# Performance work log

Measured on AMD Instinct MI355X. Metric: run time of the kernel, lower is better.

Reference implementation:

```python
import jax, jax.numpy as jnp
import numpy as np

S, B, H2 = 2048, 16, 1024   # seq_len, batch, 2*hidden_dim
H = H2 // 2                  # hidden_dim
N = 4096                     # number of spans with nonempty tags
T = 8192                     # total number of target tags (ragged, flattened)
L = 256                      # label_dim
V = 50000                    # vocab size
GAMMA = 1.0


def setup_inputs() -> dict:
    key = jax.random.key(0)
    ks = jax.random.split(key, 10)
    hidden = jax.random.normal(ks[0], (S, B, H2), jnp.float32)
    W1 = jax.random.normal(ks[1], (L, H2), jnp.float32) * (1.0 / np.sqrt(H2))
    b1 = jnp.zeros((L,), jnp.float32)
    W2 = jax.random.normal(ks[2], (V, L), jnp.float32) * (1.0 / np.sqrt(L))
    b2 = jnp.zeros((V,), jnp.float32)
    span_bid = jax.random.randint(ks[3], (N,), 0, B, jnp.int32)
    span_begin = jax.random.randint(ks[4], (N,), 0, S, jnp.int32)
    span_end = jax.random.randint(ks[5], (N,), 0, S, jnp.int32)
    tag_span_id = jax.random.randint(ks[6], (T,), 0, N, jnp.int32)
    tags = jax.random.randint(ks[7], (T,), 0, V, jnp.int32)
    return {"hidden": hidden, "W1": W1, "b1": b1, "W2": W2, "b2": b2,
            "span_bid": span_bid, "span_begin": span_begin,
            "span_end": span_end, "tag_span_id": tag_span_id, "tags": tags}


def reference(hidden, W1, b1, W2, b2, span_bid, span_begin, span_end,
              tag_span_id, tags):
    # span embedding: forward half at begin-1 (wraps like torch negative idx),
    # backward half at end.  -> [N, 2H]
    fwd = hidden[(span_begin - 1) % S, span_bid, :H]
    bwd = hidden[span_end, span_bid, H:]
    feat = jnp.concatenate([fwd, bwd], axis=-1)          # [N, 2H]
    x = jnp.tanh(feat @ W1.T + b1)                       # [N, L]  (Linear+Tanh)
    logits = x @ W2.T + b2                               # [N, V]
    logp = jax.nn.log_softmax(logits, axis=-1)           # stable softmax->log
    pos_logp = logp[tag_span_id, tags]                   # [T] gathered targets
    pos = jnp.exp(pos_logp)                              # positive_probs
    # focal loss, gamma=1: -(1-p)^gamma * log(p), summed over all tags
    loss = jnp.sum(-((1.0 - pos) ** GAMMA) * pos_logp)
    loss = loss / (jnp.float32(T) + 1e-5)
    return loss.reshape(1)
```

## Files before the change

kernel.cpp:

```cpp
#include <hip/hip_runtime.h>
#include <hip/hip_fp8.h>

#define S_    2048
#define B_    16
#define H2_   1024
#define H_    512
#define N_    4096
#define T_    8192
#define L_    256
#define V_    50000
#define VPAD_ 50048

#define LOG2E_ 1.44269504088896f

typedef float  floatx4 __attribute__((ext_vector_type(4)));
typedef __bf16 bf16x8  __attribute__((ext_vector_type(8)));
typedef int    intx4   __attribute__((ext_vector_type(4)));
typedef int    intx8   __attribute__((ext_vector_type(8)));

__device__ inline unsigned short f2bf(float f) {
  unsigned u = __builtin_bit_cast(unsigned, f);
  unsigned r = u + 0x7fffu + ((u >> 16) & 1u);
  return (unsigned short)(r >> 16);
}
__device__ inline float bf2f(unsigned short s) {
  unsigned u = ((unsigned)s) << 16;
  return __builtin_bit_cast(float, u);
}
__device__ inline unsigned char f2fp8(float f) {
  return (unsigned char)__hip_cvt_float_to_fp8(f, __HIP_SATFINITE, __HIP_E4M3);
}

__device__ inline void stage16(const void* g, void* l) {
  __builtin_amdgcn_global_load_lds(
      (const __attribute__((address_space(1))) void*)g,
      (__attribute__((address_space(3))) void*)l, 16, 0, 0);
}

__global__ __launch_bounds__(256) void gather_k(
    const float* __restrict__ hidden, const int* __restrict__ sbid,
    const int* __restrict__ sbeg, const int* __restrict__ send,
    unsigned short* __restrict__ featbf, float* __restrict__ lse) {
  const int n = blockIdx.x;
  const int t = threadIdx.x;
  if (t == 0) lse[n] = 0.f;
  if (n == 0 && t == 1) lse[N_] = 0.f;
  if (n == 0 && t == 2) ((unsigned*)lse)[N_ + 1] = 0u;
  const int bid = sbid[n];
  int r = sbeg[n] - 1; if (r < 0) r += S_;
  const int e = send[n];
  const size_t fbase = (size_t)r * (B_ * H2_) + (size_t)bid * H2_;
  const size_t bbase = (size_t)e * (B_ * H2_) + (size_t)bid * H2_;
  const int c = t * 4;
  const float4 v = (t < 128) ? *reinterpret_cast<const float4*>(hidden + fbase + c)
                             : *reinterpret_cast<const float4*>(hidden + bbase + c);
  unsigned short o[4];
  o[0] = f2bf(v.x); o[1] = f2bf(v.y); o[2] = f2bf(v.z); o[3] = f2bf(v.w);
  *reinterpret_cast<unsigned long long*>(featbf + (size_t)n * H2_ + c) =
      *reinterpret_cast<unsigned long long*>(o);
}

__global__ __launch_bounds__(256) void convert_k(
    const float* __restrict__ W1, const float* __restrict__ W2,
    const float* __restrict__ b2, unsigned short* __restrict__ w1b,
    unsigned char* __restrict__ w2f8, float* __restrict__ ebp) {
  const int gid = blockIdx.x * 256 + threadIdx.x;
  const int gstride = gridDim.x * 256;
  for (long j = (long)gid * 8; j < (long)VPAD_ * 256; j += (long)gstride * 8) {
    int row = (int)(j >> 8);
    unsigned char o[8];
    if (row < V_) {
#pragma unroll
      for (int q = 0; q < 8; q++) o[q] = f2fp8(W2[j + q] * LOG2E_);
    } else {
#pragma unroll
      for (int q = 0; q < 8; q++) o[q] = 0;
    }
    *reinterpret_cast<unsigned long long*>(w2f8 + j) =
        *reinterpret_cast<unsigned long long*>(o);
  }
  for (int j = gid; j < L_ * H2_; j += gstride) w1b[j] = f2bf(W1[j]);
  for (int j = gid; j < VPAD_; j += gstride) ebp[j] = (j < V_) ? __expf(b2[j]) : 0.f;
}

__global__ __launch_bounds__(256) void gemm1_k(
    const unsigned short* __restrict__ A,
    const unsigned short* __restrict__ Bw,
    const float* __restrict__ b1,
    unsigned short* __restrict__ xbf,
    unsigned char* __restrict__ xf8) {
  __shared__ __align__(16) unsigned short sA[64 * 64];
  __shared__ __align__(16) unsigned short sB[64 * 64];
  const int tid   = threadIdx.x;
  const int mtile = (int)(blockIdx.x >> 2) * 64;
  const int ntile = (int)(blockIdx.x & 3) * 64;
  const int lane = tid & 63, wave = tid >> 6;
  const int wr = (wave & 1) * 32, wc = (wave >> 1) * 32;
  const int fr = lane & 15, fq = lane >> 4;
  floatx4 acc[2][2] = {};
  for (int k0 = 0; k0 < H2_; k0 += 64) {
#pragma unroll
    for (int i = 0; i < 2; i++) {
      const int slot = tid + i * 256;
      const int r = slot >> 3, cc = slot & 7;
      const int gk = cc ^ (r & 7);
      stage16(A  + (size_t)(mtile + r) * H2_ + k0 + gk * 8, &sA[slot * 8]);
      stage16(Bw + (size_t)(ntile + r) * H2_ + k0 + gk * 8, &sB[slot * 8]);
    }
    __syncthreads();
#pragma unroll
    for (int ks = 0; ks < 2; ks++) {
      bf16x8 av[2], bv[2];
#pragma unroll
      for (int mi = 0; mi < 2; mi++) {
        const int r = wr + mi * 16 + fr, kc = ks * 4 + fq;
        av[mi] = *reinterpret_cast<const bf16x8*>(&sA[(r * 8 + (kc ^ (r & 7))) * 8]);
      }
#pragma unroll
      for (int ni = 0; ni < 2; ni++) {
        const int r = wc + ni * 16 + fr, kc = ks * 4 + fq;
        bv[ni] = *reinterpret_cast<const bf16x8*>(&sB[(r * 8 + (kc ^ (r & 7))) * 8]);
      }
#pragma unroll
      for (int mi = 0; mi < 2; mi++)
#pragma unroll
        for (int ni = 0; ni < 2; ni++)
          acc[mi][ni] = __builtin_amdgcn_mfma_f32_16x16x32_bf16(av[mi], bv[ni], acc[mi][ni], 0, 0, 0);
    }
    __syncthreads();
  }
#pragma unroll
  for (int ni = 0; ni < 2; ni++) {
    const int col = ntile + wc + ni * 16 + fr;
    const float bias = b1[col];
#pragma unroll
    for (int mi = 0; mi < 2; mi++)
#pragma unroll
      for (int r = 0; r < 4; r++) {
        const int row = mtile + wr + mi * 16 + fq * 4 + r;
        const float t = tanhf(acc[mi][ni][r] + bias);
        xbf[(size_t)row * L_ + col] = f2bf(t);
        xf8[(size_t)row * L_ + col] = f2fp8(t);
      }
  }
}

__global__ __launch_bounds__(512, 4) void gemm2_k(
    const unsigned char* __restrict__ X8,
    const unsigned char* __restrict__ W8,
    const float* __restrict__ ebp,
    float* __restrict__ lse_sum) {
  __shared__ __align__(16) unsigned char sB[2][32768];
  const int tid   = threadIdx.x;
  const int mtile = ((int)blockIdx.x >> 4) * 128;
  const int strip = (int)blockIdx.x & 15;
  const int vt0   = (strip < 7) ? strip * 25 : 175 + (strip - 7) * 24;
  const int nt    = (strip < 7) ? 25 : 24;
  const int lane = tid & 63, wave = tid >> 6;
  const int wr = (wave & 3) * 32;
  const int wc = (wave >> 2) * 64;
  const int fr = lane & 15, fq = lane >> 4;

#pragma unroll
  for (int i = 0; i < 4; i++) {
    const int slot = tid + i * 512;
    const int r = slot >> 4, c = slot & 15;
    stage16(X8 + (size_t)(mtile + r) * 256 + ((c ^ (r & 15)) << 4), &sB[0][slot << 4]);
  }
  __syncthreads();
  intx8 af[2][2];
#pragma unroll
  for (int mi = 0; mi < 2; mi++)
#pragma unroll
    for (int kh = 0; kh < 2; kh++) {
      const int r  = wr + mi * 16 + fr;
      const int c0 = kh * 8 + fq * 2;
      *reinterpret_cast<intx4*>(&af[mi][kh]) =
          *reinterpret_cast<const intx4*>(&sB[0][(r << 8) + ((c0 ^ (r & 15)) << 4)]);
      *(reinterpret_cast<intx4*>(&af[mi][kh]) + 1) =
          *reinterpret_cast<const intx4*>(&sB[0][(r << 8) + (((c0 + 1) ^ (r & 15)) << 4)]);
    }
  __syncthreads();

  float sacc[2][4];
#pragma unroll
  for (int mi = 0; mi < 2; mi++)
#pragma unroll
    for (int r = 0; r < 4; r++) sacc[mi][r] = 0.f;

  float eb_cur[4], eb_nxt[4];
#pragma unroll
  for (int ni = 0; ni < 4; ni++)
    eb_nxt[ni] = ebp[vt0 * 128 + wc + ni * 16 + fr];
  {
    const unsigned char* base = W8 + (size_t)vt0 * 128 * 256;
#pragma unroll
    for (int i = 0; i < 4; i++) {
      const int slot = tid + i * 512;
      const int r = slot >> 4, c = slot & 15;
      stage16(base + ((size_t)r << 8) + ((c ^ (r & 15)) << 4), &sB[0][slot << 4]);
    }
  }

  for (int j = 0; j < nt; j++) {
#pragma unroll
    for (int ni = 0; ni < 4; ni++) eb_cur[ni] = eb_nxt[ni];
    __syncthreads();
    if (j + 1 < nt) {
      const int vt = vt0 + j + 1;
#pragma unroll
      for (int ni = 0; ni < 4; ni++)
        eb_nxt[ni] = ebp[vt * 128 + wc + ni * 16 + fr];
      const unsigned char* base = W8 + (size_t)vt * 128 * 256;
      unsigned char* dst = &sB[(j + 1) & 1][0];
#pragma unroll
      for (int i = 0; i < 4; i++) {
        const int slot = tid + i * 512;
        const int r = slot >> 4, c = slot & 15;
        stage16(base + ((size_t)r << 8) + ((c ^ (r & 15)) << 4), dst + (slot << 4));
      }
    }

    const unsigned char* bb = &sB[j & 1][0];
    floatx4 acc[2][4] = {};
#pragma unroll
    for (int ni = 0; ni < 4; ni++) {
      __builtin_amdgcn_s_setprio(1);
#pragma unroll
      for (int kh = 0; kh < 2; kh++) {
        intx8 bv;
        const int r  = wc + ni * 16 + fr;
        const int c0 = kh * 8 + fq * 2;
        *reinterpret_cast<intx4*>(&bv) =
            *reinterpret_cast<const intx4*>(&bb[(r << 8) + ((c0 ^ (r & 15)) << 4)]);
        *(reinterpret_cast<intx4*>(&bv) + 1) =
            *reinterpret_cast<const intx4*>(&bb[(r << 8) + (((c0 + 1) ^ (r & 15)) << 4)]);
#pragma unroll
        for (int mi = 0; mi < 2; mi++)
          acc[mi][ni] = __builtin_amdgcn_mfma_scale_f32_16x16x128_f8f6f4(
              af[mi][kh], bv, acc[mi][ni], 0, 0,
              0, 0x7f7f7f7f, 0, 0x7f7f7f7f);
      }
      __builtin_amdgcn_s_setprio(0);
      if (ni > 0) {
        const int pi = ni - 1;
#pragma unroll
        for (int mi = 0; mi < 2; mi++)
#pragma unroll
          for (int r = 0; r < 4; r++)
            sacc[mi][r] = fmaf(eb_cur[pi], __builtin_amdgcn_exp2f(acc[mi][pi][r]),
                               sacc[mi][r]);
      }
    }
#pragma unroll
    for (int mi = 0; mi < 2; mi++)
#pragma unroll
      for (int r = 0; r < 4; r++)
        sacc[mi][r] = fmaf(eb_cur[3], __builtin_amdgcn_exp2f(acc[mi][3][r]),
                           sacc[mi][r]);
  }

#pragma unroll
  for (int mi = 0; mi < 2; mi++)
#pragma unroll
    for (int r = 0; r < 4; r++) {
      float s = sacc[mi][r];
      s += __shfl_xor(s, 1);
      s += __shfl_xor(s, 2);
      s += __shfl_xor(s, 4);
      s += __shfl_xor(s, 8);
      if (fr == 0)
        atomicAdd(&lse_sum[mtile + wr + mi * 16 + fq * 4 + r], s);
    }
}

__global__ __launch_bounds__(256) void loss_k(
    const unsigned short* __restrict__ xbf, const float* __restrict__ W2,
    const float* __restrict__ b2, const int* __restrict__ tsid,
    const int* __restrict__ tags, const float* __restrict__ lse_sum,
    float* __restrict__ loss_acc, unsigned* __restrict__ ticket,
    float* __restrict__ out) {
  const int lane = threadIdx.x & 63;
  const int gw = (int)(blockIdx.x * 256 + threadIdx.x) >> 6;
  const int nw = (int)(gridDim.x * 256) >> 6;
  float total = 0.f;
  for (int t = gw; t < T_; t += nw) {
    const int sid = tsid[t];
    const int v   = tags[t];
    const unsigned short* xr = xbf + (size_t)sid * L_;
    const float* w2r = W2 + (size_t)v * L_;
    float d = 0.f;
#pragma unroll
    for (int q = 0; q < 4; q++) {
      const int j = lane * 4 + q;
      d += bf2f(xr[j]) * w2r[j];
    }
#pragma unroll
    for (int m = 1; m < 64; m <<= 1) d += __shfl_xor(d, m);
    const float lp  = d + b2[v] - logf(lse_sum[sid]);
    const float pos = __expf(lp);
    total += (pos - 1.f) * lp;
  }
  if (lane == 0) atomicAdd(loss_acc, total);
  __syncthreads();
  __threadfence();
  if (threadIdx.x == 0) {
    const unsigned t = atomicAdd(ticket, 1u);
    if (t == (unsigned)gridDim.x - 1u) {
      const float v = atomicAdd(loss_acc, 0.0f);
      out[0] = v / (8192.0f + 1e-5f);
    }
  }
}

extern "C" void kernel_launch(void* const* d_in, const int* in_sizes, int n_in,
                              void* d_out, int out_size, void* d_ws, size_t ws_size,
                              hipStream_t stream) {
  const float* hidden = (const float*)d_in[0];
  const float* W1     = (const float*)d_in[1];
  const float* b1     = (const float*)d_in[2];
  const float* W2     = (const float*)d_in[3];
  const float* b2     = (const float*)d_in[4];
  const int* sbid = (const int*)d_in[5];
  const int* sbeg = (const int*)d_in[6];
  const int* send = (const int*)d_in[7];
  const int* tsid = (const int*)d_in[8];
  const int* tags = (const int*)d_in[9];
  float* out = (float*)d_out;

  char* ws = (char*)d_ws;
  unsigned short* featbf = (unsigned short*)(ws);
  unsigned short* xbf    = (unsigned short*)(ws + 8388608);
  unsigned short* w1bf   = (unsigned short*)(ws + 10485760);
  unsigned char*  xf8    = (unsigned char*) (ws + 11010048);
  unsigned char*  w2f8   = (unsigned char*) (ws + 12058624);
  float* ebp  = (float*)(ws + 24870912);
  float* lse  = (float*)(ws + 25071104);
  float* lacc = lse + N_;
  unsigned* ticket = (unsigned*)(lse + N_ + 1);

  gather_k<<<dim3(N_), dim3(256), 0, stream>>>(hidden, sbid, sbeg, send, featbf, lse);
  convert_k<<<dim3(4096), dim3(256), 0, stream>>>(W1, W2, b2, w1bf, w2f8, ebp);
  gemm1_k<<<dim3(256), dim3(256), 0, stream>>>(featbf, w1bf, b1, xbf, xf8);
  gemm2_k<<<dim3(512), dim3(512), 0, stream>>>(xf8, w2f8, ebp, lse);
  loss_k<<<dim3(256), dim3(256), 0, stream>>>(xbf, W2, b2, tsid, tags, lse, lacc, ticket, out);
}
```

Baseline: 310.6 us.

## Double-buffer gemm1 LDS tiles, grid-stride gather, vectorize loss loads

gemm1 now uses two LDS buffers, so the next K tile is prefetched while the current one feeds the MFMAs, and one barrier per iteration is dropped. gather_k becomes a grid-stride loop over 512 blocks instead of one block per span. loss_k loads x and W2 rows with single vector loads and launches 512 blocks. These reduce load latency and launch overhead in small kernels, at the cost of double the LDS in gemm1.

```diff
diff --git a/kernel.cpp b/kernel.cpp
--- a/kernel.cpp
+++ b/kernel.cpp
@@ -41,23 +41,26 @@
     const float* __restrict__ hidden, const int* __restrict__ sbid,
     const int* __restrict__ sbeg, const int* __restrict__ send,
     unsigned short* __restrict__ featbf, float* __restrict__ lse) {
-  const int n = blockIdx.x;
   const int t = threadIdx.x;
-  if (t == 0) lse[n] = 0.f;
-  if (n == 0 && t == 1) lse[N_] = 0.f;
-  if (n == 0 && t == 2) ((unsigned*)lse)[N_ + 1] = 0u;
-  const int bid = sbid[n];
-  int r = sbeg[n] - 1; if (r < 0) r += S_;
-  const int e = send[n];
-  const size_t fbase = (size_t)r * (B_ * H2_) + (size_t)bid * H2_;
-  const size_t bbase = (size_t)e * (B_ * H2_) + (size_t)bid * H2_;
-  const int c = t * 4;
-  const float4 v = (t < 128) ? *reinterpret_cast<const float4*>(hidden + fbase + c)
-                             : *reinterpret_cast<const float4*>(hidden + bbase + c);
-  unsigned short o[4];
-  o[0] = f2bf(v.x); o[1] = f2bf(v.y); o[2] = f2bf(v.z); o[3] = f2bf(v.w);
-  *reinterpret_cast<unsigned long long*>(featbf + (size_t)n * H2_ + c) =
-      *reinterpret_cast<unsigned long long*>(o);
+  if (blockIdx.x == 0 && t == 0) {
+    lse[N_] = 0.f;
+    ((unsigned*)lse)[N_ + 1] = 0u;
+  }
+  for (int n = blockIdx.x; n < N_; n += gridDim.x) {
+    if (t == 0) lse[n] = 0.f;
+    const int bid = sbid[n];
+    int r = sbeg[n] - 1; if (r < 0) r += S_;
+    const int e = send[n];
+    const size_t fbase = (size_t)r * (B_ * H2_) + (size_t)bid * H2_;
+    const size_t bbase = (size_t)e * (B_ * H2_) + (size_t)bid * H2_;
+    const int c = t * 4;
+    const float4 v = (t < 128) ? *reinterpret_cast<const float4*>(hidden + fbase + c)
+                               : *reinterpret_cast<const float4*>(hidden + bbase + c);
+    unsigned short o[4];
+    o[0] = f2bf(v.x); o[1] = f2bf(v.y); o[2] = f2bf(v.z); o[3] = f2bf(v.w);
+    *reinterpret_cast<unsigned long long*>(featbf + (size_t)n * H2_ + c) =
+        *reinterpret_cast<unsigned long long*>(o);
+  }
 }
 
 __global__ __launch_bounds__(256) void convert_k(
@@ -89,8 +92,8 @@
     const float* __restrict__ b1,
     unsigned short* __restrict__ xbf,
     unsigned char* __restrict__ xf8) {
-  __shared__ __align__(16) unsigned short sA[64 * 64];
-  __shared__ __align__(16) unsigned short sB[64 * 64];
+  __shared__ __align__(16) unsigned short sA[2][64 * 64];
+  __shared__ __align__(16) unsigned short sB[2][64 * 64];
   const int tid   = threadIdx.x;
   const int mtile = (int)(blockIdx.x >> 2) * 64;
   const int ntile = (int)(blockIdx.x & 3) * 64;
@@ -98,28 +101,42 @@
   const int wr = (wave & 1) * 32, wc = (wave >> 1) * 32;
   const int fr = lane & 15, fq = lane >> 4;
   floatx4 acc[2][2] = {};
-  for (int k0 = 0; k0 < H2_; k0 += 64) {
-#pragma unroll
-    for (int i = 0; i < 2; i++) {
-      const int slot = tid + i * 256;
-      const int r = slot >> 3, cc = slot & 7;
-      const int gk = cc ^ (r & 7);
-      stage16(A  + (size_t)(mtile + r) * H2_ + k0 + gk * 8, &sA[slot * 8]);
-      stage16(Bw + (size_t)(ntile + r) * H2_ + k0 + gk * 8, &sB[slot * 8]);
-    }
+
+#pragma unroll
+  for (int i = 0; i < 2; i++) {
+    const int slot = tid + i * 256;
+    const int r = slot >> 3, cc = slot & 7;
+    const int gk = cc ^ (r & 7);
+    stage16(A  + (size_t)(mtile + r) * H2_ + gk * 8, &sA[0][slot * 8]);
+    stage16(Bw + (size_t)(ntile + r) * H2_ + gk * 8, &sB[0][slot * 8]);
+  }
+
+  for (int kt = 0; kt < 16; kt++) {
+    const int cur = kt & 1;
     __syncthreads();
+    if (kt + 1 < 16) {
+      const int k0 = (kt + 1) * 64;
+#pragma unroll
+      for (int i = 0; i < 2; i++) {
+        const int slot = tid + i * 256;
+        const int r = slot >> 3, cc = slot & 7;
+        const int gk = cc ^ (r & 7);
+        stage16(A  + (size_t)(mtile + r) * H2_ + k0 + gk * 8, &sA[cur ^ 1][slot * 8]);
+        stage16(Bw + (size_t)(ntile + r) * H2_ + k0 + gk * 8, &sB[cur ^ 1][slot * 8]);
+      }
+    }
 #pragma unroll
     for (int ks = 0; ks < 2; ks++) {
       bf16x8 av[2], bv[2];
 #pragma unroll
       for (int mi = 0; mi < 2; mi++) {
         const int r = wr + mi * 16 + fr, kc = ks * 4 + fq;
-        av[mi] = *reinterpret_cast<const bf16x8*>(&sA[(r * 8 + (kc ^ (r & 7))) * 8]);
+        av[mi] = *reinterpret_cast<const bf16x8*>(&sA[cur][(r * 8 + (kc ^ (r & 7))) * 8]);
       }
 #pragma unroll
       for (int ni = 0; ni < 2; ni++) {
         const int r = wc + ni * 16 + fr, kc = ks * 4 + fq;
-        bv[ni] = *reinterpret_cast<const bf16x8*>(&sB[(r * 8 + (kc ^ (r & 7))) * 8]);
+        bv[ni] = *reinterpret_cast<const bf16x8*>(&sB[cur][(r * 8 + (kc ^ (r & 7))) * 8]);
       }
 #pragma unroll
       for (int mi = 0; mi < 2; mi++)
@@ -127,7 +144,6 @@
         for (int ni = 0; ni < 2; ni++)
           acc[mi][ni] = __builtin_amdgcn_mfma_f32_16x16x32_bf16(av[mi], bv[ni], acc[mi][ni], 0, 0, 0);
     }
-    __syncthreads();
   }
 #pragma unroll
   for (int ni = 0; ni < 2; ni++) {
@@ -289,12 +305,13 @@
     const int v   = tags[t];
     const unsigned short* xr = xbf + (size_t)sid * L_;
     const float* w2r = W2 + (size_t)v * L_;
-    float d = 0.f;
-#pragma unroll
-    for (int q = 0; q < 4; q++) {
-      const int j = lane * 4 + q;
-      d += bf2f(xr[j]) * w2r[j];
-    }
+    const unsigned long long xv =
+        *reinterpret_cast<const unsigned long long*>(xr + (lane << 2));
+    const float4 wv = *reinterpret_cast<const float4*>(w2r + (lane << 2));
+    float d = bf2f((unsigned short)xv) * wv.x
+            + bf2f((unsigned short)(xv >> 16)) * wv.y
+            + bf2f((unsigned short)(xv >> 32)) * wv.z
+            + bf2f((unsigned short)(xv >> 48)) * wv.w;
 #pragma unroll
     for (int m = 1; m < 64; m <<= 1) d += __shfl_xor(d, m);
     const float lp  = d + b2[v] - logf(lse_sum[sid]);
@@ -339,9 +356,9 @@
   float* lacc = lse + N_;
   unsigned* ticket = (unsigned*)(lse + N_ + 1);
 
-  gather_k<<<dim3(N_), dim3(256), 0, stream>>>(hidden, sbid, sbeg, send, featbf, lse);
+  gather_k<<<dim3(512), dim3(256), 0, stream>>>(hidden, sbid, sbeg, send, featbf, lse);
   convert_k<<<dim3(4096), dim3(256), 0, stream>>>(W1, W2, b2, w1bf, w2f8, ebp);
   gemm1_k<<<dim3(256), dim3(256), 0, stream>>>(featbf, w1bf, b1, xbf, xf8);
   gemm2_k<<<dim3(512), dim3(512), 0, stream>>>(xf8, w2f8, ebp, lse);
-  loss_k<<<dim3(256), dim3(256), 0, stream>>>(xbf, W2, b2, tsid, tags, lse, lacc, ticket, out);
-}
+  loss_k<<<dim3(512), dim3(256), 0, stream>>>(xbf, W2, b2, tsid, tags, lse, lacc, ticket, out);
+}
```

New measurement: 339.2 us. +9.2%, slower.
